# Kernel tuning notes

Hardware: AMD Instinct MI355X
Metric: run time of the kernel (lower is better)

## Reference

```python
import jax, jax.numpy as jnp
import numpy as np

B, S, HID, HEADS, INTER = 64, 512, 40, 4, 20
DH = HID // HEADS  # 10
EPS = 1e-5


def layer_norm(x, g, b):
    mu = jnp.mean(x, axis=-1, keepdims=True)
    var = jnp.mean(jnp.square(x - mu), axis=-1, keepdims=True)
    return (x - mu) * jax.lax.rsqrt(var + EPS) * g + b


def setup_inputs() -> dict:
    key = jax.random.key(0)
    ks = jax.random.split(key, 16)
    s = 0.05
    return {
        "hidden_states": jax.random.normal(ks[0], (B, S, HID), jnp.float32),
        "ln1_g": jnp.ones((HID,), jnp.float32),
        "ln1_b": jnp.zeros((HID,), jnp.float32),
        "Wq": jax.random.normal(ks[1], (HID, HID), jnp.float32) * s,
        "bq": jnp.zeros((HID,), jnp.float32),
        "Wk": jax.random.normal(ks[2], (HID, HID), jnp.float32) * s,
        "bk": jnp.zeros((HID,), jnp.float32),
        "Wv": jax.random.normal(ks[3], (HID, HID), jnp.float32) * s,
        "bv": jnp.zeros((HID,), jnp.float32),
        "Wo": jax.random.normal(ks[4], (HID, HID), jnp.float32) * s,
        "bo": jnp.zeros((HID,), jnp.float32),
        "ln2_g": jnp.ones((HID,), jnp.float32),
        "ln2_b": jnp.zeros((HID,), jnp.float32),
        "W1": jax.random.normal(ks[5], (HID, INTER), jnp.float32) * s,
        "b1": jnp.zeros((INTER,), jnp.float32),
        "W2": jax.random.normal(ks[6], (INTER, HID), jnp.float32) * s,
        "b2": jnp.zeros((HID,), jnp.float32),
    }


def reference(hidden_states, ln1_g, ln1_b, Wq, bq, Wk, bk, Wv, bv, Wo, bo,
              ln2_g, ln2_b, W1, b1, W2, b2):
    x = hidden_states
    # --- self-attention (pre-LN) ---
    h = layer_norm(x, ln1_g, ln1_b)
    q = (h @ Wq + bq).reshape(B, S, HEADS, DH)
    k = (h @ Wk + bk).reshape(B, S, HEADS, DH)
    v = (h @ Wv + bv).reshape(B, S, HEADS, DH)
    # scores: [B, H, S, S]
    scores = jnp.einsum('bqhd,bkhd->bhqk', q, k) / jnp.sqrt(jnp.float32(DH))
    probs = jax.nn.softmax(scores, axis=-1)
    ctx = jnp.einsum('bhqk,bkhd->bqhd', probs, v).reshape(B, S, HID)
    attn_out = ctx @ Wo + bo + x
    # --- FFN (pre-LN) ---
    h2 = layer_norm(attn_out, ln2_g, ln2_b)
    inter = jax.nn.gelu(h2 @ W1 + b1, approximate=False)
    out = inter @ W2 + b2 + attn_out
    return out
```

## Files before the change

### kernel.cpp

```cpp
#include <hip/hip_runtime.h>
#include <stdint.h>

#define EPSF 1e-5f

typedef __attribute__((ext_vector_type(8)))  short bh8;
typedef __attribute__((ext_vector_type(16))) float fx16;
typedef __attribute__((ext_vector_type(4)))  int   i32x4;

__device__ __forceinline__ int cvtpk(float a, float b) {
    int r;
    asm("v_cvt_pk_bf16_f32 %0, %1, %2" : "=v"(r) : "v"(a), "v"(b));
    return r;
}
__device__ __forceinline__ float fastrcp(float x) {
    float r;
    asm("v_rcp_f32 %0, %1" : "=v"(r) : "v"(x));
    return r;
}

__global__ __launch_bounds__(256) void k_ln_qkv(
    const float* __restrict__ x, const float* __restrict__ g, const float* __restrict__ be,
    const float* __restrict__ Wq, const float* __restrict__ bq,
    const float* __restrict__ Wk, const float* __restrict__ bk,
    const float* __restrict__ Wv, const float* __restrict__ bv,
    unsigned short* __restrict__ qo, unsigned short* __restrict__ ko,
    unsigned short* __restrict__ vt)
{
    __shared__ float sX[64][41];

    const int tid = threadIdx.x;
    const float4* xblk = (const float4*)(x + (size_t)blockIdx.x * 64 * 40);
    for (int idx = tid; idx < 640; idx += 256) {
        float4 u = xblk[idx];
        int fl = idx * 4;
        int r = fl / 40, c = fl - r * 40;
        sX[r][c] = u.x; sX[r][c + 1] = u.y; sX[r][c + 2] = u.z; sX[r][c + 3] = u.w;
    }
    __syncthreads();

    const int lane = tid & 63;
    const int part = tid >> 6;
    const int hp = __builtin_amdgcn_readfirstlane(part);

    float s1 = 0.f, s2 = 0.f;
#pragma unroll 8
    for (int i = 0; i < 40; i++) { float v = sX[lane][i]; s1 += v; s2 += v * v; }
    const float mu = s1 * 0.025f;
    const float rs = rsqrtf(s2 * 0.025f - mu * mu + EPSF);

    float hrow[40];
#pragma unroll 4
    for (int i = 0; i < 40; i++)
        hrow[i] = (sX[lane][i] - mu) * rs * g[i] + be[i];

    const float* Wp[3] = {Wq, Wk, Wv};
    const float* Bp[3] = {bq, bk, bv};

    float acc[3][10];
#pragma unroll
    for (int w = 0; w < 3; w++)
#pragma unroll
        for (int c = 0; c < 10; c++) acc[w][c] = Bp[w][hp * 10 + c];

#pragma unroll 2
    for (int i = 0; i < 40; i++) {
        const float hi = hrow[i];
#pragma unroll
        for (int w = 0; w < 3; w++) {
            const float* wp = Wp[w] + i * 40 + hp * 10;
#pragma unroll
            for (int c = 0; c < 10; c++) acc[w][c] += hi * wp[c];
        }
    }

    const float cs = 1.4426950408889634f / 3.1622776601683795f;
#pragma unroll
    for (int c = 0; c < 10; c++) acc[0][c] *= cs;

    const int row0 = blockIdx.x * 64;
    const int b4 = (row0 >> 9) * 4, s0 = row0 & 511;
    const size_t srow = (size_t)(b4 + hp) * 512 + s0 + lane;

    {
        int p0 = cvtpk(acc[0][0], acc[0][1]);
        int p1 = cvtpk(acc[0][2], acc[0][3]);
        int p2 = cvtpk(acc[0][4], acc[0][5]);
        int p3 = cvtpk(acc[0][6], acc[0][7]);
        int p4 = cvtpk(acc[0][8], acc[0][9]);
        i32x4* dst = (i32x4*)qo + srow * 2;
        dst[0] = (i32x4){p0, p1, p2, p3};
        dst[1] = (i32x4){p4, 0, 0, 0};
    }
    {
        int p0 = cvtpk(acc[1][0], acc[1][1]);
        int p1 = cvtpk(acc[1][2], acc[1][3]);
        int p2 = cvtpk(acc[1][4], acc[1][5]);
        int p3 = cvtpk(acc[1][6], acc[1][7]);
        int p4 = cvtpk(acc[1][8], acc[1][9]);
        i32x4* dst = (i32x4*)ko + srow * 2;
        dst[0] = (i32x4){p0, p1, p2, p3};
        dst[1] = (i32x4){p4, 0, 0, 0};
    }
    {
        int p0 = cvtpk(acc[2][0], acc[2][1]);
        int p1 = cvtpk(acc[2][2], acc[2][3]);
        int p2 = cvtpk(acc[2][4], acc[2][5]);
        int p3 = cvtpk(acc[2][6], acc[2][7]);
        int p4 = cvtpk(acc[2][8], acc[2][9]);
        unsigned short* vb = vt + ((size_t)(b4 + hp) * 16) * 512 + (s0 + lane);
        vb[0 * 512] = (unsigned short)(p0 & 0xffff);
        vb[1 * 512] = (unsigned short)((unsigned)p0 >> 16);
        vb[2 * 512] = (unsigned short)(p1 & 0xffff);
        vb[3 * 512] = (unsigned short)((unsigned)p1 >> 16);
        vb[4 * 512] = (unsigned short)(p2 & 0xffff);
        vb[5 * 512] = (unsigned short)((unsigned)p2 >> 16);
        vb[6 * 512] = (unsigned short)(p3 & 0xffff);
        vb[7 * 512] = (unsigned short)((unsigned)p3 >> 16);
        vb[8 * 512] = (unsigned short)(p4 & 0xffff);
        vb[9 * 512] = (unsigned short)((unsigned)p4 >> 16);
        vb[10 * 512] = 0x3F80;
        vb[11 * 512] = 0; vb[12 * 512] = 0; vb[13 * 512] = 0;
        vb[14 * 512] = 0; vb[15 * 512] = 0;
    }
}

__global__ __launch_bounds__(512) void k_attn(
    const unsigned short* __restrict__ qg, const unsigned short* __restrict__ kg,
    const unsigned short* __restrict__ vt, float* __restrict__ ctx)
{
    __shared__ __align__(16) char smem[16640];

    const int tid = threadIdx.x;
    const int bh = blockIdx.x;
    const int lane = tid & 63;
    const int wavei = tid >> 6;

    bh8 qf0, qf1;
    {
        const char* qp = (const char*)qg + (size_t)bh * 512 * 32;
        const int qbase = wavei * 64;
        qf0 = *(const bh8*)(qp + (size_t)(qbase + (lane & 31)) * 32 + (lane >> 5) * 16);
        qf1 = *(const bh8*)(qp + (size_t)(qbase + 32 + (lane & 31)) * 32 + (lane >> 5) * 16);
    }
    {
        const i32x4* gv = (const i32x4*)((const char*)vt + (size_t)bh * 16 * 1024);
        for (int c = tid; c < 1024; c += 512) {
            i32x4 u = gv[c];
            *(i32x4*)(smem + (c >> 6) * 1040 + (c & 63) * 16) = u;
        }
    }
    __syncthreads();

    const char* sV = smem;
    const int krow = lane & 31, khalf = lane >> 5;
    const int vrow = lane & 15;
    const bool vzero = (lane & 16) != 0;

    const bh8* gk = (const bh8*)((const char*)kg + (size_t)bh * 512 * 32);

    fx16 acc0 = (fx16)(0.0f), acc1 = (fx16)(0.0f);

    bh8 kf = gk[(size_t)krow * 2 + khalf];
    for (int kt = 0; kt < 16; ++kt) {
        bh8 kfn = kf;
        if (kt < 15) kfn = gk[(size_t)((kt + 1) * 32 + krow) * 2 + khalf];
        bh8 vf0 = *(const bh8*)(sV + vrow * 1040 + kt * 64 + khalf * 16);
        bh8 vf1 = *(const bh8*)(sV + vrow * 1040 + kt * 64 + 32 + khalf * 16);
        if (vzero) { vf0 = (bh8)(short)0; vf1 = (bh8)(short)0; }
#pragma unroll
        for (int qt = 0; qt < 2; ++qt) {
            fx16 s = __builtin_amdgcn_mfma_f32_32x32x16_bf16(
                kf, qt ? qf1 : qf0, (fx16)(0.0f), 0, 0, 0);
            float e[16];
#pragma unroll
            for (int r = 0; r < 16; ++r) e[r] = __builtin_amdgcn_exp2f(s[r]);
            int c0 = cvtpk(e[0], e[1]),   c1 = cvtpk(e[2], e[3]);
            int c2 = cvtpk(e[4], e[5]),   c3 = cvtpk(e[6], e[7]);
            int c4 = cvtpk(e[8], e[9]),   c5 = cvtpk(e[10], e[11]);
            int c6 = cvtpk(e[12], e[13]), c7 = cvtpk(e[14], e[15]);
            asm("v_permlane32_swap_b32 %0, %1" : "+v"(c0), "+v"(c2));
            asm("v_permlane32_swap_b32 %0, %1" : "+v"(c1), "+v"(c3));
            asm("v_permlane32_swap_b32 %0, %1" : "+v"(c4), "+v"(c6));
            asm("v_permlane32_swap_b32 %0, %1" : "+v"(c5), "+v"(c7));
            union { i32x4 i; bh8 h; } lo, hi;
            lo.i = (i32x4){c0, c1, c2, c3};
            hi.i = (i32x4){c4, c5, c6, c7};
            if (qt == 0) {
                acc0 = __builtin_amdgcn_mfma_f32_32x32x16_bf16(lo.h, vf0, acc0, 0, 0, 0);
                acc0 = __builtin_amdgcn_mfma_f32_32x32x16_bf16(hi.h, vf1, acc0, 0, 0, 0);
            } else {
                acc1 = __builtin_amdgcn_mfma_f32_32x32x16_bf16(lo.h, vf0, acc1, 0, 0, 0);
                acc1 = __builtin_amdgcn_mfma_f32_32x32x16_bf16(hi.h, vf1, acc1, 0, 0, 0);
            }
        }
        kf = kfn;
    }

    const int d = lane & 31;
    const int qb = wavei * 64;
#pragma unroll
    for (int qt = 0; qt < 2; ++qt) {
        fx16 A = qt ? acc1 : acc0;
#pragma unroll
        for (int r = 0; r < 16; ++r) {
            float v = A[r];
            float ls = __shfl(v, (lane & 32) | 10, 64);
            float o = v * fastrcp(ls);
            if (d < 10) {
                int q = qb + qt * 32 + (r & 3) + 8 * (r >> 2) + 4 * (lane >> 5);
                ctx[((size_t)bh * 512 + q) * 10 + d] = o;
            }
        }
    }
}

__global__ __launch_bounds__(256) void k_out_ffn(
    const float* __restrict__ ctx, const float* __restrict__ x,
    const float* __restrict__ Wo, const float* __restrict__ bo,
    const float* __restrict__ g2, const float* __restrict__ bt2,
    const float* __restrict__ W1, const float* __restrict__ b1,
    const float* __restrict__ W2, const float* __restrict__ b2,
    float* __restrict__ out)
{
    __shared__ float sWo[40][48];
    __shared__ float sW1[40][32];
    __shared__ float sW2[20][48];
    __shared__ float sBo[40], sG2[40], sBt2[40], sB1[20], sB2[40];
    __shared__ float sCtx[64][41];
    __shared__ float sH[64][41];
    __shared__ float sIt[64][21];
    __shared__ float sSum[64][4], sSum2[64][4];

    const int tid = threadIdx.x;
    for (int idx = tid; idx < 1600; idx += 256) {
        int i = idx / 40, j = idx % 40;
        sWo[i][(j / 10) * 12 + (j % 10)] = Wo[idx];
    }
    for (int idx = tid; idx < 800; idx += 256) {
        {
            int i = idx / 20, j = idx % 20;
            sW1[i][(j / 5) * 8 + (j % 5)] = W1[idx];
        }
        {
            int i = idx / 40, j = idx % 40;
            sW2[i][(j / 10) * 12 + (j % 10)] = W2[idx];
        }
    }
    if (tid < 40) { sBo[tid] = bo[tid]; sG2[tid] = g2[tid]; sBt2[tid] = bt2[tid]; sB2[tid] = b2[tid]; }
    if (tid < 20) sB1[tid] = b1[tid];

    const int row0 = blockIdx.x * 64;
    const int b = row0 >> 9, s0 = row0 & 511;

    for (int idx = tid; idx < 640; idx += 256) {
        const int hh = idx / 160, f = idx - hh * 160;
        float4 u = *(const float4*)(ctx + ((size_t)((b * 4 + hh) * 512 + s0)) * 10 + f * 4);
        const int fo = f * 4;
        float e[4] = {u.x, u.y, u.z, u.w};
#pragma unroll
        for (int t = 0; t < 4; t++) {
            const int fe = fo + t;
            const int r = fe / 10, c = fe - r * 10;
            sCtx[r][hh * 10 + c] = e[t];
        }
    }
    const float4* xblk = (const float4*)(x + (size_t)blockIdx.x * 64 * 40);
    for (int idx = tid; idx < 640; idx += 256) {
        float4 w = xblk[idx];
        int fl = idx * 4;
        int r = fl / 40, c = fl - r * 40;
        sH[r][c] = w.x; sH[r][c + 1] = w.y; sH[r][c + 2] = w.z; sH[r][c + 3] = w.w;
    }
    __syncthreads();

    const int lane = tid & 63;
    const int wv = tid >> 6;
    const int j0 = wv * 10;

    float acc[10];
#pragma unroll
    for (int j = 0; j < 10; j++) acc[j] = sBo[j0 + j] + sH[lane][j0 + j];
#pragma unroll 8
    for (int i = 0; i < 40; i++) {
        const float ci = sCtx[lane][i];
        const float4* wrow = (const float4*)&sWo[i][wv * 12];
        float4 w0 = wrow[0], w1 = wrow[1], w2 = wrow[2];
        acc[0] += ci * w0.x; acc[1] += ci * w0.y; acc[2] += ci * w0.z; acc[3] += ci * w0.w;
        acc[4] += ci * w1.x; acc[5] += ci * w1.y; acc[6] += ci * w1.z; acc[7] += ci * w1.w;
        acc[8] += ci * w2.x; acc[9] += ci * w2.y;
    }
    {
        float s1 = 0.f, s2 = 0.f;
#pragma unroll
        for (int j = 0; j < 10; j++) { s1 += acc[j]; s2 += acc[j] * acc[j]; }
        sSum[lane][wv] = s1; sSum2[lane][wv] = s2;
    }
    __syncthreads();
    const float mu = (sSum[lane][0] + sSum[lane][1] + sSum[lane][2] + sSum[lane][3]) * 0.025f;
    const float ex2 = (sSum2[lane][0] + sSum2[lane][1] + sSum2[lane][2] + sSum2[lane][3]) * 0.025f;
    const float rs = rsqrtf(ex2 - mu * mu + EPSF);
#pragma unroll
    for (int j = 0; j < 10; j++)
        sH[lane][j0 + j] = (acc[j] - mu) * rs * sG2[j0 + j] + sBt2[j0 + j];
    __syncthreads();

    const int f0 = wv * 5;
    float it[5];
#pragma unroll
    for (int j = 0; j < 5; j++) it[j] = sB1[f0 + j];
#pragma unroll 8
    for (int i = 0; i < 40; i++) {
        const float hi = sH[lane][i];
        const float4* wrow = (const float4*)&sW1[i][wv * 8];
        float4 w0 = wrow[0], w1 = wrow[1];
        it[0] += hi * w0.x; it[1] += hi * w0.y; it[2] += hi * w0.z; it[3] += hi * w0.w;
        it[4] += hi * w1.x;
    }
#pragma unroll
    for (int j = 0; j < 5; j++) {
        float t = it[j];
        sIt[lane][f0 + j] = 0.5f * t * (1.0f + erff(t * 0.70710678118654752f));
    }
    __syncthreads();

    float o[10];
#pragma unroll
    for (int j = 0; j < 10; j++) o[j] = acc[j] + sB2[j0 + j];
#pragma unroll 4
    for (int i = 0; i < 20; i++) {
        const float ii = sIt[lane][i];
        const float4* wrow = (const float4*)&sW2[i][wv * 12];
        float4 w0 = wrow[0], w1 = wrow[1], w2 = wrow[2];
        o[0] += ii * w0.x; o[1] += ii * w0.y; o[2] += ii * w0.z; o[3] += ii * w0.w;
        o[4] += ii * w1.x; o[5] += ii * w1.y; o[6] += ii * w1.z; o[7] += ii * w1.w;
        o[8] += ii * w2.x; o[9] += ii * w2.y;
    }
#pragma unroll
    for (int j = 0; j < 10; j++) sCtx[lane][j0 + j] = o[j];
    __syncthreads();

    float4* oblk = (float4*)(out + (size_t)blockIdx.x * 64 * 40);
    for (int idx = tid; idx < 640; idx += 256) {
        int fl = idx * 4;
        int r = fl / 40, c = fl - r * 40;
        float4 u;
        u.x = sCtx[r][c]; u.y = sCtx[r][c + 1]; u.z = sCtx[r][c + 2]; u.w = sCtx[r][c + 3];
        oblk[idx] = u;
    }
}

extern "C" void kernel_launch(void* const* d_in, const int* in_sizes, int n_in,
                              void* d_out, int out_size, void* d_ws, size_t ws_size,
                              hipStream_t stream)
{
    const float* x   = (const float*)d_in[0];
    const float* g1  = (const float*)d_in[1];
    const float* be1 = (const float*)d_in[2];
    const float* Wq  = (const float*)d_in[3];
    const float* bq  = (const float*)d_in[4];
    const float* Wk  = (const float*)d_in[5];
    const float* bk  = (const float*)d_in[6];
    const float* Wv  = (const float*)d_in[7];
    const float* bv  = (const float*)d_in[8];
    const float* Wo  = (const float*)d_in[9];
    const float* bo  = (const float*)d_in[10];
    const float* g2  = (const float*)d_in[11];
    const float* bt2 = (const float*)d_in[12];
    const float* W1  = (const float*)d_in[13];
    const float* b1  = (const float*)d_in[14];
    const float* W2  = (const float*)d_in[15];
    const float* b2  = (const float*)d_in[16];

    unsigned short* wsu = (unsigned short*)d_ws;
    const size_t T = (size_t)256 * 512 * 16;
    unsigned short* q  = wsu;
    unsigned short* k  = wsu + T;
    unsigned short* vt = wsu + 2 * T;
    float* ctx = (float*)(wsu + 3 * T);

    k_ln_qkv<<<512, 256, 0, stream>>>(x, g1, be1, Wq, bq, Wk, bk, Wv, bv, q, k, vt);
    k_attn<<<256, 512, 0, stream>>>(q, k, vt, ctx);
    k_out_ffn<<<512, 256, 0, stream>>>(ctx, x, Wo, bo, g2, bt2, W1, b1, W2, b2,
                                       (float*)d_out);
}
```

Before: 138.7 us.

## Fuse LayerNorm+QKV projection into attention kernel, keeping Q/K/V in LDS

Merges the LN1+QKV projection kernel with the attention kernel, so each (batch, head) block normalises all 512 rows of its batch and computes that head's Q, K and V directly into shared memory. This removes the global-memory round trip for the bf16 Q/K/V tensors and one kernel launch. In exchange, LayerNorm and projection work is repeated four times per batch, once per head. The block also needs about 82 KB of LDS, which limits occupancy to a single block per CU.

```diff
diff --git a/kernel.cpp b/kernel.cpp
--- a/kernel.cpp
+++ b/kernel.cpp
@@ -18,154 +18,121 @@
     return r;
 }
 
-__global__ __launch_bounds__(256) void k_ln_qkv(
+__global__ __launch_bounds__(512) void k_qkv_attn(
     const float* __restrict__ x, const float* __restrict__ g, const float* __restrict__ be,
     const float* __restrict__ Wq, const float* __restrict__ bq,
     const float* __restrict__ Wk, const float* __restrict__ bk,
     const float* __restrict__ Wv, const float* __restrict__ bv,
-    unsigned short* __restrict__ qo, unsigned short* __restrict__ ko,
-    unsigned short* __restrict__ vt)
+    float* __restrict__ ctx)
 {
-    __shared__ float sX[64][41];
+    __shared__ __align__(16) char smem[83968];
 
     const int tid = threadIdx.x;
-    const float4* xblk = (const float4*)(x + (size_t)blockIdx.x * 64 * 40);
-    for (int idx = tid; idx < 640; idx += 256) {
-        float4 u = xblk[idx];
-        int fl = idx * 4;
-        int r = fl / 40, c = fl - r * 40;
-        sX[r][c] = u.x; sX[r][c + 1] = u.y; sX[r][c + 2] = u.z; sX[r][c + 3] = u.w;
-    }
-    __syncthreads();
-
+    const int bh = blockIdx.x;
+    const int b  = bh >> 2;
+    const int h  = bh & 3;
     const int lane = tid & 63;
-    const int part = tid >> 6;
-    const int hp = __builtin_amdgcn_readfirstlane(part);
+    const int wavei = tid >> 6;
+
+    float* sX = (float*)smem;
+    {
+        const float4* xb = (const float4*)(x + (size_t)b * 512 * 40);
+        for (int idx = tid; idx < 5120; idx += 512) {
+            float4 u = xb[idx];
+            int fl = idx * 4;
+            int r = fl / 40, c = fl - r * 40;
+            sX[r * 41 + c] = u.x; sX[r * 41 + c + 1] = u.y;
+            sX[r * 41 + c + 2] = u.z; sX[r * 41 + c + 3] = u.w;
+        }
+    }
+    __syncthreads();
 
     float s1 = 0.f, s2 = 0.f;
 #pragma unroll 8
-    for (int i = 0; i < 40; i++) { float v = sX[lane][i]; s1 += v; s2 += v * v; }
+    for (int i = 0; i < 40; i++) { float v = sX[tid * 41 + i]; s1 += v; s2 += v * v; }
     const float mu = s1 * 0.025f;
     const float rs = rsqrtf(s2 * 0.025f - mu * mu + EPSF);
 
     float hrow[40];
 #pragma unroll 4
     for (int i = 0; i < 40; i++)
-        hrow[i] = (sX[lane][i] - mu) * rs * g[i] + be[i];
-
-    const float* Wp[3] = {Wq, Wk, Wv};
-    const float* Bp[3] = {bq, bk, bv};
-
-    float acc[3][10];
-#pragma unroll
-    for (int w = 0; w < 3; w++)
-#pragma unroll
-        for (int c = 0; c < 10; c++) acc[w][c] = Bp[w][hp * 10 + c];
-
+        hrow[i] = (sX[tid * 41 + i] - mu) * rs * g[i] + be[i];
+
+    float aq[10], ak[10], av[10];
+#pragma unroll
+    for (int c = 0; c < 10; c++) {
+        aq[c] = bq[h * 10 + c]; ak[c] = bk[h * 10 + c]; av[c] = bv[h * 10 + c];
+    }
 #pragma unroll 2
     for (int i = 0; i < 40; i++) {
         const float hi = hrow[i];
-#pragma unroll
-        for (int w = 0; w < 3; w++) {
-            const float* wp = Wp[w] + i * 40 + hp * 10;
-#pragma unroll
-            for (int c = 0; c < 10; c++) acc[w][c] += hi * wp[c];
-        }
-    }
-
+        const float* wq = Wq + i * 40 + h * 10;
+        const float* wk = Wk + i * 40 + h * 10;
+        const float* wv = Wv + i * 40 + h * 10;
+#pragma unroll
+        for (int c = 0; c < 10; c++) {
+            aq[c] += hi * wq[c]; ak[c] += hi * wk[c]; av[c] += hi * wv[c];
+        }
+    }
     const float cs = 1.4426950408889634f / 3.1622776601683795f;
 #pragma unroll
-    for (int c = 0; c < 10; c++) acc[0][c] *= cs;
-
-    const int row0 = blockIdx.x * 64;
-    const int b4 = (row0 >> 9) * 4, s0 = row0 & 511;
-    const size_t srow = (size_t)(b4 + hp) * 512 + s0 + lane;
-
-    {
-        int p0 = cvtpk(acc[0][0], acc[0][1]);
-        int p1 = cvtpk(acc[0][2], acc[0][3]);
-        int p2 = cvtpk(acc[0][4], acc[0][5]);
-        int p3 = cvtpk(acc[0][6], acc[0][7]);
-        int p4 = cvtpk(acc[0][8], acc[0][9]);
-        i32x4* dst = (i32x4*)qo + srow * 2;
-        dst[0] = (i32x4){p0, p1, p2, p3};
-        dst[1] = (i32x4){p4, 0, 0, 0};
-    }
-    {
-        int p0 = cvtpk(acc[1][0], acc[1][1]);
-        int p1 = cvtpk(acc[1][2], acc[1][3]);
-        int p2 = cvtpk(acc[1][4], acc[1][5]);
-        int p3 = cvtpk(acc[1][6], acc[1][7]);
-        int p4 = cvtpk(acc[1][8], acc[1][9]);
-        i32x4* dst = (i32x4*)ko + srow * 2;
-        dst[0] = (i32x4){p0, p1, p2, p3};
-        dst[1] = (i32x4){p4, 0, 0, 0};
-    }
-    {
-        int p0 = cvtpk(acc[2][0], acc[2][1]);
-        int p1 = cvtpk(acc[2][2], acc[2][3]);
-        int p2 = cvtpk(acc[2][4], acc[2][5]);
-        int p3 = cvtpk(acc[2][6], acc[2][7]);
-        int p4 = cvtpk(acc[2][8], acc[2][9]);
-        unsigned short* vb = vt + ((size_t)(b4 + hp) * 16) * 512 + (s0 + lane);
-        vb[0 * 512] = (unsigned short)(p0 & 0xffff);
-        vb[1 * 512] = (unsigned short)((unsigned)p0 >> 16);
-        vb[2 * 512] = (unsigned short)(p1 & 0xffff);
-        vb[3 * 512] = (unsigned short)((unsigned)p1 >> 16);
-        vb[4 * 512] = (unsigned short)(p2 & 0xffff);
-        vb[5 * 512] = (unsigned short)((unsigned)p2 >> 16);
-        vb[6 * 512] = (unsigned short)(p3 & 0xffff);
-        vb[7 * 512] = (unsigned short)((unsigned)p3 >> 16);
-        vb[8 * 512] = (unsigned short)(p4 & 0xffff);
-        vb[9 * 512] = (unsigned short)((unsigned)p4 >> 16);
-        vb[10 * 512] = 0x3F80;
-        vb[11 * 512] = 0; vb[12 * 512] = 0; vb[13 * 512] = 0;
-        vb[14 * 512] = 0; vb[15 * 512] = 0;
-    }
-}
-
-__global__ __launch_bounds__(512) void k_attn(
-    const unsigned short* __restrict__ qg, const unsigned short* __restrict__ kg,
-    const unsigned short* __restrict__ vt, float* __restrict__ ctx)
-{
-    __shared__ __align__(16) char smem[16640];
-
-    const int tid = threadIdx.x;
-    const int bh = blockIdx.x;
-    const int lane = tid & 63;
-    const int wavei = tid >> 6;
-
-    bh8 qf0, qf1;
-    {
-        const char* qp = (const char*)qg + (size_t)bh * 512 * 32;
-        const int qbase = wavei * 64;
-        qf0 = *(const bh8*)(qp + (size_t)(qbase + (lane & 31)) * 32 + (lane >> 5) * 16);
-        qf1 = *(const bh8*)(qp + (size_t)(qbase + 32 + (lane & 31)) * 32 + (lane >> 5) * 16);
-    }
-    {
-        const i32x4* gv = (const i32x4*)((const char*)vt + (size_t)bh * 16 * 1024);
-        for (int c = tid; c < 1024; c += 512) {
-            i32x4 u = gv[c];
-            *(i32x4*)(smem + (c >> 6) * 1040 + (c & 63) * 16) = u;
-        }
-    }
-    __syncthreads();
-
-    const char* sV = smem;
+    for (int c = 0; c < 10; c++) aq[c] *= cs;
+
+    __syncthreads();
+
+    char* sK  = smem;
+    char* sVT = smem + 24576;
+    char* sQ  = smem + 41216;
+    {
+        int p0 = cvtpk(ak[0], ak[1]), p1 = cvtpk(ak[2], ak[3]);
+        int p2 = cvtpk(ak[4], ak[5]), p3 = cvtpk(ak[6], ak[7]);
+        int p4 = cvtpk(ak[8], ak[9]);
+        i32x4* kd = (i32x4*)(sK + tid * 48);
+        kd[0] = (i32x4){p0, p1, p2, p3};
+        kd[1] = (i32x4){p4, 0, 0, 0};
+    }
+    {
+        int p0 = cvtpk(aq[0], aq[1]), p1 = cvtpk(aq[2], aq[3]);
+        int p2 = cvtpk(aq[4], aq[5]), p3 = cvtpk(aq[6], aq[7]);
+        int p4 = cvtpk(aq[8], aq[9]);
+        i32x4* qd = (i32x4*)(sQ + tid * 32);
+        qd[0] = (i32x4){p0, p1, p2, p3};
+        qd[1] = (i32x4){p4, 0, 0, 0};
+    }
+    {
+        int p0 = cvtpk(av[0], av[1]), p1 = cvtpk(av[2], av[3]);
+        int p2 = cvtpk(av[4], av[5]), p3 = cvtpk(av[6], av[7]);
+        int p4 = cvtpk(av[8], av[9]);
+        unsigned short* vb = (unsigned short*)sVT + tid;
+        vb[0 * 520] = (unsigned short)(p0 & 0xffff);
+        vb[1 * 520] = (unsigned short)((unsigned)p0 >> 16);
+        vb[2 * 520] = (unsigned short)(p1 & 0xffff);
+        vb[3 * 520] = (unsigned short)((unsigned)p1 >> 16);
+        vb[4 * 520] = (unsigned short)(p2 & 0xffff);
+        vb[5 * 520] = (unsigned short)((unsigned)p2 >> 16);
+        vb[6 * 520] = (unsigned short)(p3 & 0xffff);
+        vb[7 * 520] = (unsigned short)((unsigned)p3 >> 16);
+        vb[8 * 520] = (unsigned short)(p4 & 0xffff);
+        vb[9 * 520] = (unsigned short)((unsigned)p4 >> 16);
+        vb[10 * 520] = 0x3F80;
+        vb[11 * 520] = 0; vb[12 * 520] = 0; vb[13 * 520] = 0;
+        vb[14 * 520] = 0; vb[15 * 520] = 0;
+    }
+    __syncthreads();
+
     const int krow = lane & 31, khalf = lane >> 5;
     const int vrow = lane & 15;
     const bool vzero = (lane & 16) != 0;
 
-    const bh8* gk = (const bh8*)((const char*)kg + (size_t)bh * 512 * 32);
+    bh8 qf0 = *(const bh8*)(sQ + (size_t)(wavei * 64 + (lane & 31)) * 32 + (lane >> 5) * 16);
+    bh8 qf1 = *(const bh8*)(sQ + (size_t)(wavei * 64 + 32 + (lane & 31)) * 32 + (lane >> 5) * 16);
 
     fx16 acc0 = (fx16)(0.0f), acc1 = (fx16)(0.0f);
 
-    bh8 kf = gk[(size_t)krow * 2 + khalf];
     for (int kt = 0; kt < 16; ++kt) {
-        bh8 kfn = kf;
-        if (kt < 15) kfn = gk[(size_t)((kt + 1) * 32 + krow) * 2 + khalf];
-        bh8 vf0 = *(const bh8*)(sV + vrow * 1040 + kt * 64 + khalf * 16);
-        bh8 vf1 = *(const bh8*)(sV + vrow * 1040 + kt * 64 + 32 + khalf * 16);
+        bh8 kf  = *(const bh8*)(sK + (kt * 32 + krow) * 48 + khalf * 16);
+        bh8 vf0 = *(const bh8*)(sVT + vrow * 1040 + kt * 64 + khalf * 16);
+        bh8 vf1 = *(const bh8*)(sVT + vrow * 1040 + kt * 64 + 32 + khalf * 16);
         if (vzero) { vf0 = (bh8)(short)0; vf1 = (bh8)(short)0; }
 #pragma unroll
         for (int qt = 0; qt < 2; ++qt) {
@@ -193,7 +160,6 @@
                 acc1 = __builtin_amdgcn_mfma_f32_32x32x16_bf16(hi.h, vf1, acc1, 0, 0, 0);
             }
         }
-        kf = kfn;
     }
 
     const int d = lane & 31;
@@ -371,15 +337,9 @@
     const float* W2  = (const float*)d_in[15];
     const float* b2  = (const float*)d_in[16];
 
-    unsigned short* wsu = (unsigned short*)d_ws;
-    const size_t T = (size_t)256 * 512 * 16;
-    unsigned short* q  = wsu;
-    unsigned short* k  = wsu + T;
-    unsigned short* vt = wsu + 2 * T;
-    float* ctx = (float*)(wsu + 3 * T);
-
-    k_ln_qkv<<<512, 256, 0, stream>>>(x, g1, be1, Wq, bq, Wk, bk, Wv, bv, q, k, vt);
-    k_attn<<<256, 512, 0, stream>>>(q, k, vt, ctx);
+    float* ctx = (float*)d_ws;
+
+    k_qkv_attn<<<256, 512, 0, stream>>>(x, g1, be1, Wq, bq, Wk, bk, Wv, bv, ctx);
     k_out_ffn<<<512, 256, 0, stream>>>(ctx, x, Wo, bo, g2, bt2, W1, b1, W2, b2,
                                        (float*)d_out);
 }
```

New measurement: 129.3 us, median of 2. 1.07x faster.
